# Performance work log

Hardware: AMD Instinct MI355X
Metric: run time of the kernel (lower is better)

Reference implementation:

```python
import jax, jax.numpy as jnp
import numpy as np

N_NODES = 50000
N_EDGES = 800000
D_IN = 96
D_OUT = 96


def setup_inputs() -> dict:
    key = jax.random.key(0)
    k1, k2, k3 = jax.random.split(key, 3)
    x = jax.random.normal(k1, (N_NODES, D_IN), dtype=jnp.float32)
    edge_index = jax.random.randint(k2, (2, N_EDGES), 0, N_NODES, dtype=jnp.int64)
    edge_weight = jnp.ones((N_EDGES,), dtype=jnp.float32)
    # Glorot-ish init for the linear weight, zero bias (as in PyG GCNConv)
    W = jax.random.normal(k3, (D_IN, D_OUT), dtype=jnp.float32) * (1.0 / np.sqrt(D_IN))
    b = jnp.zeros((D_OUT,), dtype=jnp.float32)
    return {"x": x, "edge_index": edge_index, "edge_weight": edge_weight, "W": W, "b": b}


def reference(x, edge_index, edge_weight, W, b):
    """PyG GCNConv: out = D^{-1/2} (A + I) D^{-1/2} (x @ W) + b."""
    N = x.shape[0]
    row, col = edge_index[0], edge_index[1]  # source -> target
    # add self loops with weight 1 (PyG default add_self_loops=True)
    loop = jnp.arange(N, dtype=edge_index.dtype)
    row = jnp.concatenate([row, loop])
    col = jnp.concatenate([col, loop])
    ew = jnp.concatenate([edge_weight, jnp.ones((N,), dtype=edge_weight.dtype)])
    # symmetric normalization based on (weighted) in-degree over col
    deg = jax.ops.segment_sum(ew, col, num_segments=N)  # [N]
    dinv = jnp.where(deg > 0, jax.lax.rsqrt(deg), 0.0)
    norm = dinv[row] * ew * dinv[col]  # [E+N]
    # linear transform first (small GEMM), then gather-scale-scatter over edges
    h = x @ W  # [N, D_OUT]
    msg = h[row] * norm[:, None]  # [E+N, D_OUT]
    out = jax.ops.segment_sum(msg, col, num_segments=N)  # [N, D_OUT]
    return out + b
```

## Files before the change

kernel.cpp:

```cpp
#include <hip/hip_runtime.h>

#define N_NODES 50000
#define N_EDGES 800000
#define D 96
#define NBKT 512
#define BNODES 98
#define BCAP 2304
#define PART_B 250
#define EPB 3200
#define EPT 13
#define CAP 48
#define NSLOT (BNODES * CAP)
#define GCAP 768

typedef float vfloat4 __attribute__((ext_vector_type(4)));

__device__ __forceinline__ float bf_lo(unsigned u) { return __uint_as_float(u << 16); }
__device__ __forceinline__ float bf_hi(unsigned u) { return __uint_as_float(u & 0xFFFF0000u); }
__device__ __forceinline__ unsigned f2bf_bits(unsigned u) {
    return (u + 0x7FFFu + ((u >> 16) & 1u)) & 0xFFFF0000u;
}
__device__ __forceinline__ unsigned short f2bf16(float f) {
    return (unsigned short)(f2bf_bits(__float_as_uint(f)) >> 16);
}

__device__ __forceinline__ int exscan256(int v, int* wsum) {
    int lane = threadIdx.x & 63;
    int wave = threadIdx.x >> 6;
    int incl = v;
#pragma unroll
    for (int off = 1; off < 64; off <<= 1) {
        int t = __shfl_up(incl, off);
        if (lane >= off) incl += t;
    }
    if (lane == 63) wsum[wave] = incl;
    __syncthreads();
    int base = 0;
#pragma unroll
    for (int wv = 0; wv < 3; ++wv) base += (wv < wave) ? wsum[wv] : 0;
    return base + incl - v;
}

__global__ __launch_bounds__(256) void k_part(const int* __restrict__ row,
                                              const int* __restrict__ col,
                                              const float* __restrict__ ew,
                                              int* __restrict__ bkt_cnt,
                                              uint2* __restrict__ bktbuf) {
    __shared__ int hist[NBKT];
    __shared__ int cur[NBKT];
    int tid = threadIdx.x;
    hist[tid] = 0;
    hist[tid + 256] = 0;
    __syncthreads();
    int e0 = blockIdx.x * EPB;
    int myc[EPT];
#pragma unroll
    for (int k = 0; k < EPT; ++k) {
        int i = tid + 256 * k;
        myc[k] = (i < EPB) ? col[e0 + i] : -1;
    }
#pragma unroll
    for (int k = 0; k < EPT; ++k)
        if (myc[k] >= 0) atomicAdd(&hist[myc[k] / BNODES], 1);
    __syncthreads();
    cur[tid] = atomicAdd(&bkt_cnt[tid], hist[tid]);
    cur[tid + 256] = atomicAdd(&bkt_cnt[tid + 256], hist[tid + 256]);
    __syncthreads();
#pragma unroll
    for (int k = 0; k < EPT; ++k) {
        int i = tid + 256 * k;
        if (myc[k] >= 0) {
            int e = e0 + i;
            int c = myc[k];
            int b = c / BNODES;
            int p = atomicAdd(&cur[b], 1);
            if (p < BCAP)
                bktbuf[(size_t)b * BCAP + p] =
                    make_uint2((unsigned)row[e] | ((unsigned)(c - b * BNODES) << 16),
                               __float_as_uint(ew[e]));
        }
    }
}

__global__ __launch_bounds__(256) void k_bin(const int* __restrict__ bkt_cnt,
                                             const uint2* __restrict__ bktbuf,
                                             unsigned* __restrict__ recs,
                                             int* __restrict__ rowptr,
                                             float* __restrict__ dinv) {
    __shared__ int wsum1[4];
    __shared__ int wsum2[4];
    __shared__ int sbkt[NBKT];
    __shared__ int lcnt[BNODES];
    __shared__ int loff[256];
    __shared__ unsigned lslot[NSLOT];
    int tid = threadIdx.x;
    int b = blockIdx.x;

    int c0 = min(bkt_cnt[2 * tid], BCAP);
    int c1 = min(bkt_cnt[2 * tid + 1], BCAP);
    int ps = exscan256(c0 + c1, wsum1);
    sbkt[2 * tid] = ps;
    sbkt[2 * tid + 1] = ps + c0;
    if (tid < BNODES) lcnt[tid] = 0;
    __syncthreads();
    int gbase = sbkt[b];
    int ne = min(bkt_cnt[b], BCAP);

    for (int i = tid; i < ne; i += 256) {
        uint2 r = bktbuf[(size_t)b * BCAP + i];
        int lc = (int)(r.x >> 16);
        int p = atomicAdd(&lcnt[lc], 1);
        if (p < CAP) lslot[lc * CAP + p] = f2bf_bits(r.y) | (r.x & 0xFFFFu);
    }
    __syncthreads();

    int myv = (tid < BNODES) ? min(lcnt[tid], CAP) : 0;
    int ex2 = exscan256(myv, wsum2);
    loff[tid] = ex2;
    __syncthreads();

    for (int i = tid; i < NSLOT; i += 256) {
        int ln = i / CAP, s = i % CAP;
        if (s < min(lcnt[ln], CAP))
            recs[gbase + loff[ln] + s] = lslot[i];
    }
    int base = b * BNODES;
    if (tid < BNODES) {
        int n = base + tid;
        if (n <= N_NODES) rowptr[n] = gbase + loff[tid];
        if (n < N_NODES) {
            int cn = min(lcnt[tid], CAP);
            float d = 1.0f;
            for (int k = 0; k < cn; ++k) d += bf_hi(lslot[tid * CAP + k]);
            dinv[n] = rsqrtf(d);
        }
    }
}

__global__ __launch_bounds__(256) void k_gemm(const float* __restrict__ x,
                                              const float* __restrict__ W,
                                              const float* __restrict__ dinv,
                                              unsigned short* __restrict__ hb) {
    __shared__ float Wl[D * D];
    int tid = threadIdx.x;
    const float4* Wg4 = (const float4*)W;
    float4* Wl4 = (float4*)Wl;
    for (int i = tid; i < D * D / 4; i += 256) Wl4[i] = Wg4[i];
    __syncthreads();

    int jg = tid % 24;
    int ng = tid / 24;
    if (ng >= 10) return;
    int j = jg * 4;
    int node0 = blockIdx.x * 40 + ng * 4;

    float acc[4][4] = {};
    for (int k4 = 0; k4 < D / 4; ++k4) {
        vfloat4 xv[4];
#pragma unroll
        for (int i = 0; i < 4; ++i)
            xv[i] = __builtin_nontemporal_load(
                (const vfloat4*)&x[(node0 + i) * D + k4 * 4]);
#pragma unroll
        for (int kk = 0; kk < 4; ++kk) {
            float4 w4 = *(const float4*)&Wl[(k4 * 4 + kk) * D + j];
#pragma unroll
            for (int i = 0; i < 4; ++i) {
                float xs = (kk == 0) ? xv[i].x : (kk == 1) ? xv[i].y
                         : (kk == 2) ? xv[i].z : xv[i].w;
                acc[i][0] += xs * w4.x;
                acc[i][1] += xs * w4.y;
                acc[i][2] += xs * w4.z;
                acc[i][3] += xs * w4.w;
            }
        }
    }
#pragma unroll
    for (int i = 0; i < 4; ++i) {
        int n = node0 + i;
        float di = dinv[n];
        ushort4 pk;
        pk.x = f2bf16(acc[i][0] * di);
        pk.y = f2bf16(acc[i][1] * di);
        pk.z = f2bf16(acc[i][2] * di);
        pk.w = f2bf16(acc[i][3] * di);
        *(ushort4*)&hb[(size_t)n * D + j] = pk;
    }
}

__global__ __launch_bounds__(192) void k_gather(const int* __restrict__ rowptr,
                                                const unsigned* __restrict__ recs,
                                                const unsigned short* __restrict__ hb,
                                                const float* __restrict__ dinv,
                                                const float* __restrict__ bias,
                                                float* __restrict__ out) {
    __shared__ unsigned sre[GCAP];
    __shared__ int sptr[17];
    int tid = threadIdx.x;
    int nb = blockIdx.x * 16;

    if (tid < 17) sptr[tid] = rowptr[nb + tid];
    __syncthreads();
    int e0 = sptr[0];
    int stage = sptr[16] - e0;
    for (int i = tid; i < stage; i += 192) sre[i] = recs[e0 + i];
    __syncthreads();

    int local = tid / 12;
    int jq = tid % 12;
    int n = nb + local;
    int j = jq * 8;

    uint4 sv = *(const uint4*)(hb + (size_t)n * D + j);
    float acc[8];
    acc[0] = bf_lo(sv.x); acc[1] = bf_hi(sv.x);
    acc[2] = bf_lo(sv.y); acc[3] = bf_hi(sv.y);
    acc[4] = bf_lo(sv.z); acc[5] = bf_hi(sv.z);
    acc[6] = bf_lo(sv.w); acc[7] = bf_hi(sv.w);

    int ls = sptr[local] - e0;
    int le = sptr[local + 1] - e0;
    int idx = ls;
    for (; idx + 4 <= le; idx += 4) {
        unsigned r0 = sre[idx], r1 = sre[idx + 1], r2 = sre[idx + 2], r3 = sre[idx + 3];
        uint4 v0 = *(const uint4*)(hb + (size_t)(r0 & 0xFFFFu) * D + j);
        uint4 v1 = *(const uint4*)(hb + (size_t)(r1 & 0xFFFFu) * D + j);
        uint4 v2 = *(const uint4*)(hb + (size_t)(r2 & 0xFFFFu) * D + j);
        uint4 v3 = *(const uint4*)(hb + (size_t)(r3 & 0xFFFFu) * D + j);
        float w0 = bf_hi(r0), w1 = bf_hi(r1), w2 = bf_hi(r2), w3 = bf_hi(r3);
        acc[0] += w0 * bf_lo(v0.x); acc[1] += w0 * bf_hi(v0.x);
        acc[2] += w0 * bf_lo(v0.y); acc[3] += w0 * bf_hi(v0.y);
        acc[4] += w0 * bf_lo(v0.z); acc[5] += w0 * bf_hi(v0.z);
        acc[6] += w0 * bf_lo(v0.w); acc[7] += w0 * bf_hi(v0.w);
        acc[0] += w1 * bf_lo(v1.x); acc[1] += w1 * bf_hi(v1.x);
        acc[2] += w1 * bf_lo(v1.y); acc[3] += w1 * bf_hi(v1.y);
        acc[4] += w1 * bf_lo(v1.z); acc[5] += w1 * bf_hi(v1.z);
        acc[6] += w1 * bf_lo(v1.w); acc[7] += w1 * bf_hi(v1.w);
        acc[0] += w2 * bf_lo(v2.x); acc[1] += w2 * bf_hi(v2.x);
        acc[2] += w2 * bf_lo(v2.y); acc[3] += w2 * bf_hi(v2.y);
        acc[4] += w2 * bf_lo(v2.z); acc[5] += w2 * bf_hi(v2.z);
        acc[6] += w2 * bf_lo(v2.w); acc[7] += w2 * bf_hi(v2.w);
        acc[0] += w3 * bf_lo(v3.x); acc[1] += w3 * bf_hi(v3.x);
        acc[2] += w3 * bf_lo(v3.y); acc[3] += w3 * bf_hi(v3.y);
        acc[4] += w3 * bf_lo(v3.z); acc[5] += w3 * bf_hi(v3.z);
        acc[6] += w3 * bf_lo(v3.w); acc[7] += w3 * bf_hi(v3.w);
    }
    for (; idx < le; ++idx) {
        unsigned r0 = sre[idx];
        uint4 v0 = *(const uint4*)(hb + (size_t)(r0 & 0xFFFFu) * D + j);
        float w0 = bf_hi(r0);
        acc[0] += w0 * bf_lo(v0.x); acc[1] += w0 * bf_hi(v0.x);
        acc[2] += w0 * bf_lo(v0.y); acc[3] += w0 * bf_hi(v0.y);
        acc[4] += w0 * bf_lo(v0.z); acc[5] += w0 * bf_hi(v0.z);
        acc[6] += w0 * bf_lo(v0.w); acc[7] += w0 * bf_hi(v0.w);
    }

    float di = dinv[n];
    float4 b0 = *(const float4*)&bias[j];
    float4 b1 = *(const float4*)&bias[j + 4];
    vfloat4 o0, o1;
    o0.x = acc[0] * di + b0.x; o0.y = acc[1] * di + b0.y;
    o0.z = acc[2] * di + b0.z; o0.w = acc[3] * di + b0.w;
    o1.x = acc[4] * di + b1.x; o1.y = acc[5] * di + b1.y;
    o1.z = acc[6] * di + b1.z; o1.w = acc[7] * di + b1.w;
    __builtin_nontemporal_store(o0, (vfloat4*)&out[(size_t)n * D + j]);
    __builtin_nontemporal_store(o1, (vfloat4*)&out[(size_t)n * D + j + 4]);
}

extern "C" void kernel_launch(void* const* d_in, const int* in_sizes, int n_in,
                              void* d_out, int out_size, void* d_ws, size_t ws_size,
                              hipStream_t stream) {
    const float* x  = (const float*)d_in[0];
    const int*   ei = (const int*)d_in[1];
    const float* ew = (const float*)d_in[2];
    const float* W  = (const float*)d_in[3];
    const float* b  = (const float*)d_in[4];
    float* out = (float*)d_out;

    const int* row = ei;
    const int* col = ei + N_EDGES;

    char* p = (char*)d_ws;
    unsigned short* hb     = (unsigned short*)p;
    uint2*          bktbuf = (uint2*)p;            p += (size_t)N_NODES * D * 2;
    unsigned*       recs   = (unsigned*)p;         p += (size_t)N_EDGES * 4;
    int*            rowptr = (int*)p;              p += (size_t)(N_NODES + 16) * 4;
    float*          dinv   = (float*)p;            p += (size_t)N_NODES * 4;
    int*            bkt_cnt= (int*)p;              p += (size_t)NBKT * 4;

    (void)hipMemsetAsync(bkt_cnt, 0, NBKT * sizeof(int), stream);
    k_part  <<<PART_B, 256, 0, stream>>>(row, col, ew, bkt_cnt, bktbuf);
    k_bin   <<<NBKT, 256, 0, stream>>>(bkt_cnt, bktbuf, recs, rowptr, dinv);
    k_gemm  <<<1250, 256, 0, stream>>>(x, W, dinv, hb);
    k_gather<<<(N_NODES + 15) / 16, 192, 0, stream>>>(rowptr, recs, hb, dinv, b, out);
}
```

Before: 152.8 us.

## Stage partition writes in LDS by bucket and sort gather nodes by degree

The partition kernel now builds a local exclusive scan of the bucket histogram and writes each edge record into shared memory grouped by bucket. It then flushes the staged records so that consecutive threads write contiguous global bucket slots, in place of scattered per-edge writes. The gather kernel ranks its 16 nodes by degree so that wavefronts handle nodes of similar edge counts, which is meant to cut divergence from uneven loop trip counts. The cost is about 25KB of extra LDS in the partition kernel, which may lower occupancy, plus an extra barrier and a small ranking step.

```diff
diff --git a/kernel.cpp b/kernel.cpp
--- a/kernel.cpp
+++ b/kernel.cpp
@@ -47,7 +47,11 @@
                                               int* __restrict__ bkt_cnt,
                                               uint2* __restrict__ bktbuf) {
     __shared__ int hist[NBKT];
-    __shared__ int cur[NBKT];
+    __shared__ int lbase[NBKT];
+    __shared__ int gcur[NBKT];
+    __shared__ int lcur[NBKT];
+    __shared__ int wsum[4];
+    __shared__ uint2 stg[EPB];
     int tid = threadIdx.x;
     hist[tid] = 0;
     hist[tid + 256] = 0;
@@ -63,8 +67,15 @@
     for (int k = 0; k < EPT; ++k)
         if (myc[k] >= 0) atomicAdd(&hist[myc[k] / BNODES], 1);
     __syncthreads();
-    cur[tid] = atomicAdd(&bkt_cnt[tid], hist[tid]);
-    cur[tid + 256] = atomicAdd(&bkt_cnt[tid + 256], hist[tid + 256]);
+    int c0 = hist[2 * tid];
+    int c1 = hist[2 * tid + 1];
+    int ps = exscan256(c0 + c1, wsum);
+    lbase[2 * tid] = ps;
+    lbase[2 * tid + 1] = ps + c0;
+    lcur[2 * tid] = ps;
+    lcur[2 * tid + 1] = ps + c0;
+    gcur[2 * tid] = atomicAdd(&bkt_cnt[2 * tid], c0);
+    gcur[2 * tid + 1] = atomicAdd(&bkt_cnt[2 * tid + 1], c1);
     __syncthreads();
 #pragma unroll
     for (int k = 0; k < EPT; ++k) {
@@ -73,12 +84,19 @@
             int e = e0 + i;
             int c = myc[k];
             int b = c / BNODES;
-            int p = atomicAdd(&cur[b], 1);
-            if (p < BCAP)
-                bktbuf[(size_t)b * BCAP + p] =
-                    make_uint2((unsigned)row[e] | ((unsigned)(c - b * BNODES) << 16),
-                               __float_as_uint(ew[e]));
+            int p = atomicAdd(&lcur[b], 1);
+            stg[p] = make_uint2((unsigned)row[e] | ((unsigned)(c - b * BNODES) << 16) |
+                                    ((unsigned)b << 23),
+                                __float_as_uint(ew[e]));
         }
+    }
+    __syncthreads();
+    for (int i = tid; i < EPB; i += 256) {
+        uint2 r = stg[i];
+        int b = (int)(r.x >> 23);
+        int pos = gcur[b] + (i - lbase[b]);
+        if (pos < BCAP)
+            bktbuf[(size_t)b * BCAP + pos] = make_uint2(r.x & 0x7FFFFFu, r.y);
     }
 }
 
@@ -196,19 +214,30 @@
                                                 float* __restrict__ out) {
     __shared__ unsigned sre[GCAP];
     __shared__ int sptr[17];
+    __shared__ unsigned char perm[16];
     int tid = threadIdx.x;
     int nb = blockIdx.x * 16;
 
     if (tid < 17) sptr[tid] = rowptr[nb + tid];
     __syncthreads();
+    if (tid < 16) {
+        int di = sptr[tid + 1] - sptr[tid];
+        int rank = 0;
+#pragma unroll
+        for (int jn = 0; jn < 16; ++jn) {
+            int dj = sptr[jn + 1] - sptr[jn];
+            rank += (dj > di) || (dj == di && jn < tid);
+        }
+        perm[rank] = (unsigned char)tid;
+    }
     int e0 = sptr[0];
     int stage = sptr[16] - e0;
     for (int i = tid; i < stage; i += 192) sre[i] = recs[e0 + i];
     __syncthreads();
 
-    int local = tid / 12;
+    int pl = perm[tid / 12];
     int jq = tid % 12;
-    int n = nb + local;
+    int n = nb + pl;
     int j = jq * 8;
 
     uint4 sv = *(const uint4*)(hb + (size_t)n * D + j);
@@ -218,8 +247,8 @@
     acc[4] = bf_lo(sv.z); acc[5] = bf_hi(sv.z);
     acc[6] = bf_lo(sv.w); acc[7] = bf_hi(sv.w);
 
-    int ls = sptr[local] - e0;
-    int le = sptr[local + 1] - e0;
+    int ls = sptr[pl] - e0;
+    int le = sptr[pl + 1] - e0;
     int idx = ls;
     for (; idx + 4 <= le; idx += 4) {
         unsigned r0 = sre[idx], r1 = sre[idx + 1], r2 = sre[idx + 2], r3 = sre[idx + 3];
```

Result: slower. 157.1 us (+2.8%).

## Fuse pipeline into one cooperative persistent kernel with grid syncs

Applied to the files above, without the earlier changes.

Replaces the four launches (partition, bin, GEMM, gather) with one cooperative kernel of 1024 blocks separated by grid-wide syncs. The binning and the x@W GEMM now run concurrently on disjoint block sets, so the GEMM no longer waits on dinv: dinv scaling moves into the gather, where per-edge weights are pre-multiplied by dinv[src] when staged in shared memory. The gather also sorts the nodes of each tile by degree to balance its waves. In exchange it pays grid-sync costs and a larger shared-memory union that may limit occupancy, and it falls back to three normal launches if the cooperative launch fails.

```diff
diff --git a/kernel.cpp b/kernel.cpp
--- a/kernel.cpp
+++ b/kernel.cpp
@@ -1,4 +1,7 @@
 #include <hip/hip_runtime.h>
+#include <hip/hip_cooperative_groups.h>
+
+namespace cg = cooperative_groups;
 
 #define N_NODES 50000
 #define N_EDGES 800000
@@ -6,12 +9,13 @@
 #define NBKT 512
 #define BNODES 98
 #define BCAP 2304
-#define PART_B 250
-#define EPB 3200
-#define EPT 13
 #define CAP 48
 #define NSLOT (BNODES * CAP)
-#define GCAP 768
+#define GRID 1024
+#define NTILE 21
+#define PCAP (NTILE * CAP)
+#define NTILES ((N_NODES + NTILE - 1) / NTILE)
+#define NVB 1250
 
 typedef float vfloat4 __attribute__((ext_vector_type(4)));
 
@@ -41,230 +45,259 @@
     return base + incl - v;
 }
 
-__global__ __launch_bounds__(256) void k_part(const int* __restrict__ row,
-                                              const int* __restrict__ col,
-                                              const float* __restrict__ ew,
-                                              int* __restrict__ bkt_cnt,
-                                              uint2* __restrict__ bktbuf) {
-    __shared__ int hist[NBKT];
-    __shared__ int cur[NBKT];
+union __align__(16) SMem {
+    struct { int hist[NBKT]; int cur[NBKT]; } p1;
+    struct {
+        int sbkt[NBKT]; int lcnt[BNODES]; int loff[256];
+        unsigned lslot[NSLOT]; int wsum1[4]; int wsum2[4];
+    } p2b;
+    struct { float Wl[D * D]; } p2g;
+    struct {
+        int sptr[NTILE + 1]; uint2 sed[PCAP]; unsigned char perm[NTILE];
+    } p3;
+};
+
+__global__ __launch_bounds__(256, 4) void k_fused(
+    const int* __restrict__ row, const int* __restrict__ col,
+    const float* __restrict__ ew, const float* __restrict__ x,
+    const float* __restrict__ W, const float* __restrict__ bias,
+    int* __restrict__ bkt_cnt, uint2* __restrict__ bktbuf,
+    unsigned* __restrict__ recs, int* __restrict__ rowptr,
+    float* __restrict__ dinv, unsigned short* __restrict__ hb,
+    float* __restrict__ out, int phase) {
+    __shared__ SMem sm;
     int tid = threadIdx.x;
-    hist[tid] = 0;
-    hist[tid + 256] = 0;
-    __syncthreads();
-    int e0 = blockIdx.x * EPB;
-    int myc[EPT];
-#pragma unroll
-    for (int k = 0; k < EPT; ++k) {
-        int i = tid + 256 * k;
-        myc[k] = (i < EPB) ? col[e0 + i] : -1;
-    }
-#pragma unroll
-    for (int k = 0; k < EPT; ++k)
-        if (myc[k] >= 0) atomicAdd(&hist[myc[k] / BNODES], 1);
-    __syncthreads();
-    cur[tid] = atomicAdd(&bkt_cnt[tid], hist[tid]);
-    cur[tid + 256] = atomicAdd(&bkt_cnt[tid + 256], hist[tid + 256]);
-    __syncthreads();
-#pragma unroll
-    for (int k = 0; k < EPT; ++k) {
-        int i = tid + 256 * k;
-        if (myc[k] >= 0) {
-            int e = e0 + i;
-            int c = myc[k];
-            int b = c / BNODES;
-            int p = atomicAdd(&cur[b], 1);
-            if (p < BCAP)
-                bktbuf[(size_t)b * BCAP + p] =
-                    make_uint2((unsigned)row[e] | ((unsigned)(c - b * BNODES) << 16),
-                               __float_as_uint(ew[e]));
-        }
-    }
-}
-
-__global__ __launch_bounds__(256) void k_bin(const int* __restrict__ bkt_cnt,
-                                             const uint2* __restrict__ bktbuf,
-                                             unsigned* __restrict__ recs,
-                                             int* __restrict__ rowptr,
-                                             float* __restrict__ dinv) {
-    __shared__ int wsum1[4];
-    __shared__ int wsum2[4];
-    __shared__ int sbkt[NBKT];
-    __shared__ int lcnt[BNODES];
-    __shared__ int loff[256];
-    __shared__ unsigned lslot[NSLOT];
-    int tid = threadIdx.x;
-    int b = blockIdx.x;
-
-    int c0 = min(bkt_cnt[2 * tid], BCAP);
-    int c1 = min(bkt_cnt[2 * tid + 1], BCAP);
-    int ps = exscan256(c0 + c1, wsum1);
-    sbkt[2 * tid] = ps;
-    sbkt[2 * tid + 1] = ps + c0;
-    if (tid < BNODES) lcnt[tid] = 0;
-    __syncthreads();
-    int gbase = sbkt[b];
-    int ne = min(bkt_cnt[b], BCAP);
-
-    for (int i = tid; i < ne; i += 256) {
-        uint2 r = bktbuf[(size_t)b * BCAP + i];
-        int lc = (int)(r.x >> 16);
-        int p = atomicAdd(&lcnt[lc], 1);
-        if (p < CAP) lslot[lc * CAP + p] = f2bf_bits(r.y) | (r.x & 0xFFFFu);
-    }
-    __syncthreads();
-
-    int myv = (tid < BNODES) ? min(lcnt[tid], CAP) : 0;
-    int ex2 = exscan256(myv, wsum2);
-    loff[tid] = ex2;
-    __syncthreads();
-
-    for (int i = tid; i < NSLOT; i += 256) {
-        int ln = i / CAP, s = i % CAP;
-        if (s < min(lcnt[ln], CAP))
-            recs[gbase + loff[ln] + s] = lslot[i];
-    }
-    int base = b * BNODES;
-    if (tid < BNODES) {
-        int n = base + tid;
-        if (n <= N_NODES) rowptr[n] = gbase + loff[tid];
-        if (n < N_NODES) {
-            int cn = min(lcnt[tid], CAP);
-            float d = 1.0f;
-            for (int k = 0; k < cn; ++k) d += bf_hi(lslot[tid * CAP + k]);
-            dinv[n] = rsqrtf(d);
-        }
-    }
-}
-
-__global__ __launch_bounds__(256) void k_gemm(const float* __restrict__ x,
-                                              const float* __restrict__ W,
-                                              const float* __restrict__ dinv,
-                                              unsigned short* __restrict__ hb) {
-    __shared__ float Wl[D * D];
-    int tid = threadIdx.x;
-    const float4* Wg4 = (const float4*)W;
-    float4* Wl4 = (float4*)Wl;
-    for (int i = tid; i < D * D / 4; i += 256) Wl4[i] = Wg4[i];
-    __syncthreads();
-
-    int jg = tid % 24;
-    int ng = tid / 24;
-    if (ng >= 10) return;
-    int j = jg * 4;
-    int node0 = blockIdx.x * 40 + ng * 4;
-
-    float acc[4][4] = {};
-    for (int k4 = 0; k4 < D / 4; ++k4) {
-        vfloat4 xv[4];
-#pragma unroll
-        for (int i = 0; i < 4; ++i)
-            xv[i] = __builtin_nontemporal_load(
-                (const vfloat4*)&x[(node0 + i) * D + k4 * 4]);
-#pragma unroll
-        for (int kk = 0; kk < 4; ++kk) {
-            float4 w4 = *(const float4*)&Wl[(k4 * 4 + kk) * D + j];
-#pragma unroll
-            for (int i = 0; i < 4; ++i) {
-                float xs = (kk == 0) ? xv[i].x : (kk == 1) ? xv[i].y
-                         : (kk == 2) ? xv[i].z : xv[i].w;
-                acc[i][0] += xs * w4.x;
-                acc[i][1] += xs * w4.y;
-                acc[i][2] += xs * w4.z;
-                acc[i][3] += xs * w4.w;
-            }
-        }
-    }
-#pragma unroll
-    for (int i = 0; i < 4; ++i) {
-        int n = node0 + i;
-        float di = dinv[n];
-        ushort4 pk;
-        pk.x = f2bf16(acc[i][0] * di);
-        pk.y = f2bf16(acc[i][1] * di);
-        pk.z = f2bf16(acc[i][2] * di);
-        pk.w = f2bf16(acc[i][3] * di);
-        *(ushort4*)&hb[(size_t)n * D + j] = pk;
-    }
-}
-
-__global__ __launch_bounds__(192) void k_gather(const int* __restrict__ rowptr,
-                                                const unsigned* __restrict__ recs,
-                                                const unsigned short* __restrict__ hb,
-                                                const float* __restrict__ dinv,
-                                                const float* __restrict__ bias,
-                                                float* __restrict__ out) {
-    __shared__ unsigned sre[GCAP];
-    __shared__ int sptr[17];
-    int tid = threadIdx.x;
-    int nb = blockIdx.x * 16;
-
-    if (tid < 17) sptr[tid] = rowptr[nb + tid];
-    __syncthreads();
-    int e0 = sptr[0];
-    int stage = sptr[16] - e0;
-    for (int i = tid; i < stage; i += 192) sre[i] = recs[e0 + i];
-    __syncthreads();
-
-    int local = tid / 12;
-    int jq = tid % 12;
-    int n = nb + local;
-    int j = jq * 8;
-
-    uint4 sv = *(const uint4*)(hb + (size_t)n * D + j);
-    float acc[8];
-    acc[0] = bf_lo(sv.x); acc[1] = bf_hi(sv.x);
-    acc[2] = bf_lo(sv.y); acc[3] = bf_hi(sv.y);
-    acc[4] = bf_lo(sv.z); acc[5] = bf_hi(sv.z);
-    acc[6] = bf_lo(sv.w); acc[7] = bf_hi(sv.w);
-
-    int ls = sptr[local] - e0;
-    int le = sptr[local + 1] - e0;
-    int idx = ls;
-    for (; idx + 4 <= le; idx += 4) {
-        unsigned r0 = sre[idx], r1 = sre[idx + 1], r2 = sre[idx + 2], r3 = sre[idx + 3];
-        uint4 v0 = *(const uint4*)(hb + (size_t)(r0 & 0xFFFFu) * D + j);
-        uint4 v1 = *(const uint4*)(hb + (size_t)(r1 & 0xFFFFu) * D + j);
-        uint4 v2 = *(const uint4*)(hb + (size_t)(r2 & 0xFFFFu) * D + j);
-        uint4 v3 = *(const uint4*)(hb + (size_t)(r3 & 0xFFFFu) * D + j);
-        float w0 = bf_hi(r0), w1 = bf_hi(r1), w2 = bf_hi(r2), w3 = bf_hi(r3);
-        acc[0] += w0 * bf_lo(v0.x); acc[1] += w0 * bf_hi(v0.x);
-        acc[2] += w0 * bf_lo(v0.y); acc[3] += w0 * bf_hi(v0.y);
-        acc[4] += w0 * bf_lo(v0.z); acc[5] += w0 * bf_hi(v0.z);
-        acc[6] += w0 * bf_lo(v0.w); acc[7] += w0 * bf_hi(v0.w);
-        acc[0] += w1 * bf_lo(v1.x); acc[1] += w1 * bf_hi(v1.x);
-        acc[2] += w1 * bf_lo(v1.y); acc[3] += w1 * bf_hi(v1.y);
-        acc[4] += w1 * bf_lo(v1.z); acc[5] += w1 * bf_hi(v1.z);
-        acc[6] += w1 * bf_lo(v1.w); acc[7] += w1 * bf_hi(v1.w);
-        acc[0] += w2 * bf_lo(v2.x); acc[1] += w2 * bf_hi(v2.x);
-        acc[2] += w2 * bf_lo(v2.y); acc[3] += w2 * bf_hi(v2.y);
-        acc[4] += w2 * bf_lo(v2.z); acc[5] += w2 * bf_hi(v2.z);
-        acc[6] += w2 * bf_lo(v2.w); acc[7] += w2 * bf_hi(v2.w);
-        acc[0] += w3 * bf_lo(v3.x); acc[1] += w3 * bf_hi(v3.x);
-        acc[2] += w3 * bf_lo(v3.y); acc[3] += w3 * bf_hi(v3.y);
-        acc[4] += w3 * bf_lo(v3.z); acc[5] += w3 * bf_hi(v3.z);
-        acc[6] += w3 * bf_lo(v3.w); acc[7] += w3 * bf_hi(v3.w);
-    }
-    for (; idx < le; ++idx) {
-        unsigned r0 = sre[idx];
-        uint4 v0 = *(const uint4*)(hb + (size_t)(r0 & 0xFFFFu) * D + j);
-        float w0 = bf_hi(r0);
-        acc[0] += w0 * bf_lo(v0.x); acc[1] += w0 * bf_hi(v0.x);
-        acc[2] += w0 * bf_lo(v0.y); acc[3] += w0 * bf_hi(v0.y);
-        acc[4] += w0 * bf_lo(v0.z); acc[5] += w0 * bf_hi(v0.z);
-        acc[6] += w0 * bf_lo(v0.w); acc[7] += w0 * bf_hi(v0.w);
-    }
-
-    float di = dinv[n];
-    float4 b0 = *(const float4*)&bias[j];
-    float4 b1 = *(const float4*)&bias[j + 4];
-    vfloat4 o0, o1;
-    o0.x = acc[0] * di + b0.x; o0.y = acc[1] * di + b0.y;
-    o0.z = acc[2] * di + b0.z; o0.w = acc[3] * di + b0.w;
-    o1.x = acc[4] * di + b1.x; o1.y = acc[5] * di + b1.y;
-    o1.z = acc[6] * di + b1.z; o1.w = acc[7] * di + b1.w;
-    __builtin_nontemporal_store(o0, (vfloat4*)&out[(size_t)n * D + j]);
-    __builtin_nontemporal_store(o1, (vfloat4*)&out[(size_t)n * D + j + 4]);
+    int bid = blockIdx.x;
+
+    if (phase <= 1) {
+        int* hist = sm.p1.hist;
+        int* cur = sm.p1.cur;
+        hist[tid] = 0;
+        hist[tid + 256] = 0;
+        __syncthreads();
+        int e0 = (bid * N_EDGES) / GRID;
+        int e1 = ((bid + 1) * N_EDGES) / GRID;
+        int myc[4];
+#pragma unroll
+        for (int k = 0; k < 4; ++k) {
+            int e = e0 + tid + 256 * k;
+            myc[k] = (e < e1) ? col[e] : -1;
+        }
+#pragma unroll
+        for (int k = 0; k < 4; ++k)
+            if (myc[k] >= 0) atomicAdd(&hist[myc[k] / BNODES], 1);
+        __syncthreads();
+        {
+            int h0 = hist[tid], h1 = hist[tid + 256];
+            cur[tid] = h0 ? atomicAdd(&bkt_cnt[tid], h0) : 0;
+            cur[tid + 256] = h1 ? atomicAdd(&bkt_cnt[tid + 256], h1) : 0;
+        }
+        __syncthreads();
+#pragma unroll
+        for (int k = 0; k < 4; ++k) {
+            if (myc[k] >= 0) {
+                int e = e0 + tid + 256 * k;
+                int c = myc[k];
+                int b = c / BNODES;
+                int p = atomicAdd(&cur[b], 1);
+                if (p < BCAP)
+                    bktbuf[(size_t)b * BCAP + p] =
+                        make_uint2((unsigned)row[e] | ((unsigned)(c - b * BNODES) << 16),
+                                   __float_as_uint(ew[e]));
+            }
+        }
+    }
+    if (phase == 0) cg::this_grid().sync();
+
+    if (phase == 0 || phase == 2) {
+        if (bid < NBKT) {
+            int* sbkt = sm.p2b.sbkt;
+            int* lcnt = sm.p2b.lcnt;
+            int* loff = sm.p2b.loff;
+            unsigned* lslot = sm.p2b.lslot;
+            int c0 = min(bkt_cnt[2 * tid], BCAP);
+            int c1 = min(bkt_cnt[2 * tid + 1], BCAP);
+            int ps = exscan256(c0 + c1, sm.p2b.wsum1);
+            sbkt[2 * tid] = ps;
+            sbkt[2 * tid + 1] = ps + c0;
+            if (tid < BNODES) lcnt[tid] = 0;
+            __syncthreads();
+            int gbase = sbkt[bid];
+            int ne = min(bkt_cnt[bid], BCAP);
+
+            for (int i = tid; i < ne; i += 256) {
+                uint2 r = bktbuf[(size_t)bid * BCAP + i];
+                int lc = (int)(r.x >> 16);
+                int p = atomicAdd(&lcnt[lc], 1);
+                if (p < CAP) lslot[lc * CAP + p] = f2bf_bits(r.y) | (r.x & 0xFFFFu);
+            }
+            __syncthreads();
+
+            int myv = (tid < BNODES) ? min(lcnt[tid], CAP) : 0;
+            int ex2 = exscan256(myv, sm.p2b.wsum2);
+            loff[tid] = ex2;
+            __syncthreads();
+
+            for (int i = tid; i < NSLOT; i += 256) {
+                int ln = i / CAP, s = i % CAP;
+                if (s < min(lcnt[ln], CAP))
+                    recs[gbase + loff[ln] + s] = lslot[i];
+            }
+            int base = bid * BNODES;
+            if (tid < BNODES) {
+                int n = base + tid;
+                if (n <= N_NODES) rowptr[n] = gbase + loff[tid];
+                if (n < N_NODES) {
+                    int cn = min(lcnt[tid], CAP);
+                    float d = 1.0f;
+                    for (int k = 0; k < cn; ++k) d += bf_hi(lslot[tid * CAP + k]);
+                    dinv[n] = rsqrtf(d);
+                }
+            }
+        } else {
+            float* Wl = sm.p2g.Wl;
+            const float4* Wg4 = (const float4*)W;
+            float4* Wl4 = (float4*)Wl;
+            for (int i = tid; i < D * D / 4; i += 256) Wl4[i] = Wg4[i];
+            __syncthreads();
+            int jg = tid % 24;
+            int ng = tid / 24;
+            for (int vb = bid - NBKT; vb < NVB; vb += (GRID - NBKT)) {
+                if (ng < 10) {
+                    int j = jg * 4;
+                    int node0 = vb * 40 + ng * 4;
+                    float acc[4][4] = {};
+                    for (int k4 = 0; k4 < D / 4; ++k4) {
+                        vfloat4 xv[4];
+#pragma unroll
+                        for (int i = 0; i < 4; ++i)
+                            xv[i] = __builtin_nontemporal_load(
+                                (const vfloat4*)&x[(node0 + i) * D + k4 * 4]);
+#pragma unroll
+                        for (int kk = 0; kk < 4; ++kk) {
+                            float4 w4 = *(const float4*)&Wl[(k4 * 4 + kk) * D + j];
+#pragma unroll
+                            for (int i = 0; i < 4; ++i) {
+                                float xs = (kk == 0) ? xv[i].x : (kk == 1) ? xv[i].y
+                                         : (kk == 2) ? xv[i].z : xv[i].w;
+                                acc[i][0] += xs * w4.x;
+                                acc[i][1] += xs * w4.y;
+                                acc[i][2] += xs * w4.z;
+                                acc[i][3] += xs * w4.w;
+                            }
+                        }
+                    }
+#pragma unroll
+                    for (int i = 0; i < 4; ++i) {
+                        ushort4 pk;
+                        pk.x = f2bf16(acc[i][0]);
+                        pk.y = f2bf16(acc[i][1]);
+                        pk.z = f2bf16(acc[i][2]);
+                        pk.w = f2bf16(acc[i][3]);
+                        *(ushort4*)&hb[(size_t)(node0 + i) * D + j] = pk;
+                    }
+                }
+            }
+        }
+    }
+    if (phase == 0) cg::this_grid().sync();
+
+    if (phase == 0 || phase == 3) {
+        int* sptr = sm.p3.sptr;
+        uint2* sed = sm.p3.sed;
+        unsigned char* perm = sm.p3.perm;
+        int lg = tid / 12;
+        int jq = tid % 12;
+        int j = jq * 8;
+        for (int t = bid; t < NTILES; t += GRID) {
+            __syncthreads();
+            int nb = t * NTILE;
+            if (tid <= NTILE) sptr[tid] = rowptr[min(nb + tid, N_NODES)];
+            __syncthreads();
+            if (tid < NTILE) {
+                int dmy = sptr[tid + 1] - sptr[tid];
+                int rank = 0;
+#pragma unroll
+                for (int jn = 0; jn < NTILE; ++jn) {
+                    int dj = sptr[jn + 1] - sptr[jn];
+                    rank += (dj > dmy) || (dj == dmy && jn < tid);
+                }
+                perm[rank] = (unsigned char)tid;
+            }
+            int e0 = sptr[0];
+            int stage = sptr[NTILE] - e0;
+            for (int i = tid; i < stage; i += 256) {
+                unsigned r = recs[e0 + i];
+                int src = (int)(r & 0xFFFFu);
+                sed[i] = make_uint2((unsigned)src,
+                                    __float_as_uint(bf_hi(r) * dinv[src]));
+            }
+            __syncthreads();
+
+            int pl = (lg < NTILE) ? perm[lg] : 0;
+            int n = nb + pl;
+            bool act = (lg < NTILE) && (n < N_NODES);
+            float acc[8] = {};
+            float di = 0.f;
+            if (act) {
+                di = dinv[n];
+                uint4 sv = *(const uint4*)(hb + (size_t)n * D + j);
+                acc[0] = bf_lo(sv.x) * di; acc[1] = bf_hi(sv.x) * di;
+                acc[2] = bf_lo(sv.y) * di; acc[3] = bf_hi(sv.y) * di;
+                acc[4] = bf_lo(sv.z) * di; acc[5] = bf_hi(sv.z) * di;
+                acc[6] = bf_lo(sv.w) * di; acc[7] = bf_hi(sv.w) * di;
+            }
+            int ls = act ? (sptr[pl] - e0) : 0;
+            int le = act ? (sptr[pl + 1] - e0) : 0;
+            int idx = ls;
+            for (; idx + 4 <= le; idx += 4) {
+                uint2 ed0 = sed[idx], ed1 = sed[idx + 1];
+                uint2 ed2 = sed[idx + 2], ed3 = sed[idx + 3];
+                uint4 v0 = *(const uint4*)(hb + (size_t)ed0.x * D + j);
+                uint4 v1 = *(const uint4*)(hb + (size_t)ed1.x * D + j);
+                uint4 v2 = *(const uint4*)(hb + (size_t)ed2.x * D + j);
+                uint4 v3 = *(const uint4*)(hb + (size_t)ed3.x * D + j);
+                float w0 = __uint_as_float(ed0.y), w1 = __uint_as_float(ed1.y);
+                float w2 = __uint_as_float(ed2.y), w3 = __uint_as_float(ed3.y);
+                acc[0] += w0 * bf_lo(v0.x); acc[1] += w0 * bf_hi(v0.x);
+                acc[2] += w0 * bf_lo(v0.y); acc[3] += w0 * bf_hi(v0.y);
+                acc[4] += w0 * bf_lo(v0.z); acc[5] += w0 * bf_hi(v0.z);
+                acc[6] += w0 * bf_lo(v0.w); acc[7] += w0 * bf_hi(v0.w);
+                acc[0] += w1 * bf_lo(v1.x); acc[1] += w1 * bf_hi(v1.x);
+                acc[2] += w1 * bf_lo(v1.y); acc[3] += w1 * bf_hi(v1.y);
+                acc[4] += w1 * bf_lo(v1.z); acc[5] += w1 * bf_hi(v1.z);
+                acc[6] += w1 * bf_lo(v1.w); acc[7] += w1 * bf_hi(v1.w);
+                acc[0] += w2 * bf_lo(v2.x); acc[1] += w2 * bf_hi(v2.x);
+                acc[2] += w2 * bf_lo(v2.y); acc[3] += w2 * bf_hi(v2.y);
+                acc[4] += w2 * bf_lo(v2.z); acc[5] += w2 * bf_hi(v2.z);
+                acc[6] += w2 * bf_lo(v2.w); acc[7] += w2 * bf_hi(v2.w);
+                acc[0] += w3 * bf_lo(v3.x); acc[1] += w3 * bf_hi(v3.x);
+                acc[2] += w3 * bf_lo(v3.y); acc[3] += w3 * bf_hi(v3.y);
+                acc[4] += w3 * bf_lo(v3.z); acc[5] += w3 * bf_hi(v3.z);
+                acc[6] += w3 * bf_lo(v3.w); acc[7] += w3 * bf_hi(v3.w);
+            }
+            for (; idx < le; ++idx) {
+                uint2 ed = sed[idx];
+                uint4 v0 = *(const uint4*)(hb + (size_t)ed.x * D + j);
+                float w0 = __uint_as_float(ed.y);
+                acc[0] += w0 * bf_lo(v0.x); acc[1] += w0 * bf_hi(v0.x);
+                acc[2] += w0 * bf_lo(v0.y); acc[3] += w0 * bf_hi(v0.y);
+                acc[4] += w0 * bf_lo(v0.z); acc[5] += w0 * bf_hi(v0.z);
+                acc[6] += w0 * bf_lo(v0.w); acc[7] += w0 * bf_hi(v0.w);
+            }
+            if (act) {
+                float4 b0 = *(const float4*)&bias[j];
+                float4 b1 = *(const float4*)&bias[j + 4];
+                vfloat4 o0, o1;
+                o0.x = acc[0] * di + b0.x; o0.y = acc[1] * di + b0.y;
+                o0.z = acc[2] * di + b0.z; o0.w = acc[3] * di + b0.w;
+                o1.x = acc[4] * di + b1.x; o1.y = acc[5] * di + b1.y;
+                o1.z = acc[6] * di + b1.z; o1.w = acc[7] * di + b1.w;
+                __builtin_nontemporal_store(o0, (vfloat4*)&out[(size_t)n * D + j]);
+                __builtin_nontemporal_store(o1, (vfloat4*)&out[(size_t)n * D + j + 4]);
+            }
+        }
+    }
 }
 
 extern "C" void kernel_launch(void* const* d_in, const int* in_sizes, int n_in,
@@ -281,16 +314,31 @@
     const int* col = ei + N_EDGES;
 
     char* p = (char*)d_ws;
-    unsigned short* hb     = (unsigned short*)p;
-    uint2*          bktbuf = (uint2*)p;            p += (size_t)N_NODES * D * 2;
+    unsigned short* hb     = (unsigned short*)p;   p += (size_t)N_NODES * D * 2;
+    uint2*          bktbuf = (uint2*)p;            p += (size_t)NBKT * BCAP * 8;
     unsigned*       recs   = (unsigned*)p;         p += (size_t)N_EDGES * 4;
-    int*            rowptr = (int*)p;              p += (size_t)(N_NODES + 16) * 4;
+    int*            rowptr = (int*)p;              p += (size_t)(N_NODES + 64) * 4;
     float*          dinv   = (float*)p;            p += (size_t)N_NODES * 4;
     int*            bkt_cnt= (int*)p;              p += (size_t)NBKT * 4;
 
     (void)hipMemsetAsync(bkt_cnt, 0, NBKT * sizeof(int), stream);
-    k_part  <<<PART_B, 256, 0, stream>>>(row, col, ew, bkt_cnt, bktbuf);
-    k_bin   <<<NBKT, 256, 0, stream>>>(bkt_cnt, bktbuf, recs, rowptr, dinv);
-    k_gemm  <<<1250, 256, 0, stream>>>(x, W, dinv, hb);
-    k_gather<<<(N_NODES + 15) / 16, 192, 0, stream>>>(rowptr, recs, hb, dinv, b, out);
-}
+
+    int phase = 0;
+    void* args[] = {(void*)&row, (void*)&col, (void*)&ew, (void*)&x, (void*)&W,
+                    (void*)&b, (void*)&bkt_cnt, (void*)&bktbuf, (void*)&recs,
+                    (void*)&rowptr, (void*)&dinv, (void*)&hb, (void*)&out,
+                    (void*)&phase};
+    hipError_t err = hipLaunchCooperativeKernel((const void*)k_fused, dim3(GRID),
+                                                dim3(256), args, 0u, stream);
+    if (err != hipSuccess) {
+        hipLaunchKernelGGL(k_fused, dim3(GRID), dim3(256), 0, stream,
+                           row, col, ew, x, W, b, bkt_cnt, bktbuf, recs,
+                           rowptr, dinv, hb, out, 1);
+        hipLaunchKernelGGL(k_fused, dim3(GRID), dim3(256), 0, stream,
+                           row, col, ew, x, W, b, bkt_cnt, bktbuf, recs,
+                           rowptr, dinv, hb, out, 2);
+        hipLaunchKernelGGL(k_fused, dim3(GRID), dim3(256), 0, stream,
+                           row, col, ew, x, W, b, bkt_cnt, bktbuf, recs,
+                           rowptr, dinv, hb, out, 3);
+    }
+}
```

After: 456.5 us. 2.99x slower.

## Fuse edge partition with GEMM and move source normalization into gather

Applied to the files above, without the earlier changes.

Merges the edge-bucketing kernel and the x@W GEMM into one launch whose blocks are split by blockIdx. This lets the GEMM run concurrently with partitioning instead of waiting for dinv. The source-side dinv scaling leaves the GEMM: each edge weight is premultiplied by dinv[src] while staging in the gather kernel. hb and bktbuf no longer alias, so workspace use grows. The gather also sorts its 16 nodes by degree so that waves get balanced work, at the cost of an extra dinv gather per edge.

```diff
diff --git a/kernel.cpp b/kernel.cpp
--- a/kernel.cpp
+++ b/kernel.cpp
@@ -12,6 +12,7 @@
 #define CAP 48
 #define NSLOT (BNODES * CAP)
 #define GCAP 768
+#define GEMM_B 1250
 
 typedef float vfloat4 __attribute__((ext_vector_type(4)));
 
@@ -41,43 +42,99 @@
     return base + incl - v;
 }
 
-__global__ __launch_bounds__(256) void k_part(const int* __restrict__ row,
-                                              const int* __restrict__ col,
-                                              const float* __restrict__ ew,
-                                              int* __restrict__ bkt_cnt,
-                                              uint2* __restrict__ bktbuf) {
-    __shared__ int hist[NBKT];
-    __shared__ int cur[NBKT];
+union __align__(16) SMemPG {
+    struct { int hist[NBKT]; int cur[NBKT]; } p;
+    float Wl[D * D];
+};
+
+__global__ __launch_bounds__(256) void k_partgemm(
+    const int* __restrict__ row, const int* __restrict__ col,
+    const float* __restrict__ ew, const float* __restrict__ x,
+    const float* __restrict__ W, int* __restrict__ bkt_cnt,
+    uint2* __restrict__ bktbuf, unsigned short* __restrict__ hb) {
+    __shared__ SMemPG sm;
     int tid = threadIdx.x;
-    hist[tid] = 0;
-    hist[tid + 256] = 0;
-    __syncthreads();
-    int e0 = blockIdx.x * EPB;
-    int myc[EPT];
-#pragma unroll
-    for (int k = 0; k < EPT; ++k) {
-        int i = tid + 256 * k;
-        myc[k] = (i < EPB) ? col[e0 + i] : -1;
-    }
-#pragma unroll
-    for (int k = 0; k < EPT; ++k)
-        if (myc[k] >= 0) atomicAdd(&hist[myc[k] / BNODES], 1);
-    __syncthreads();
-    cur[tid] = atomicAdd(&bkt_cnt[tid], hist[tid]);
-    cur[tid + 256] = atomicAdd(&bkt_cnt[tid + 256], hist[tid + 256]);
-    __syncthreads();
-#pragma unroll
-    for (int k = 0; k < EPT; ++k) {
-        int i = tid + 256 * k;
-        if (myc[k] >= 0) {
-            int e = e0 + i;
-            int c = myc[k];
-            int b = c / BNODES;
-            int p = atomicAdd(&cur[b], 1);
-            if (p < BCAP)
-                bktbuf[(size_t)b * BCAP + p] =
-                    make_uint2((unsigned)row[e] | ((unsigned)(c - b * BNODES) << 16),
-                               __float_as_uint(ew[e]));
+    int bid = blockIdx.x;
+
+    if (bid < PART_B) {
+        int* hist = sm.p.hist;
+        int* cur = sm.p.cur;
+        hist[tid] = 0;
+        hist[tid + 256] = 0;
+        __syncthreads();
+        int e0 = bid * EPB;
+        int myc[EPT];
+#pragma unroll
+        for (int k = 0; k < EPT; ++k) {
+            int i = tid + 256 * k;
+            myc[k] = (i < EPB) ? col[e0 + i] : -1;
+        }
+#pragma unroll
+        for (int k = 0; k < EPT; ++k)
+            if (myc[k] >= 0) atomicAdd(&hist[myc[k] / BNODES], 1);
+        __syncthreads();
+        {
+            int h0 = hist[tid], h1 = hist[tid + 256];
+            cur[tid] = h0 ? atomicAdd(&bkt_cnt[tid], h0) : 0;
+            cur[tid + 256] = h1 ? atomicAdd(&bkt_cnt[tid + 256], h1) : 0;
+        }
+        __syncthreads();
+#pragma unroll
+        for (int k = 0; k < EPT; ++k) {
+            int i = tid + 256 * k;
+            if (myc[k] >= 0) {
+                int e = e0 + i;
+                int c = myc[k];
+                int b = c / BNODES;
+                int p = atomicAdd(&cur[b], 1);
+                if (p < BCAP)
+                    bktbuf[(size_t)b * BCAP + p] =
+                        make_uint2((unsigned)row[e] | ((unsigned)(c - b * BNODES) << 16),
+                                   __float_as_uint(ew[e]));
+            }
+        }
+    } else {
+        float* Wl = sm.Wl;
+        const float4* Wg4 = (const float4*)W;
+        float4* Wl4 = (float4*)Wl;
+        for (int i = tid; i < D * D / 4; i += 256) Wl4[i] = Wg4[i];
+        __syncthreads();
+
+        int jg = tid % 24;
+        int ng = tid / 24;
+        if (ng < 10) {
+            int j = jg * 4;
+            int node0 = (bid - PART_B) * 40 + ng * 4;
+            float acc[4][4] = {};
+            for (int k4 = 0; k4 < D / 4; ++k4) {
+                vfloat4 xv[4];
+#pragma unroll
+                for (int i = 0; i < 4; ++i)
+                    xv[i] = __builtin_nontemporal_load(
+                        (const vfloat4*)&x[(node0 + i) * D + k4 * 4]);
+#pragma unroll
+                for (int kk = 0; kk < 4; ++kk) {
+                    float4 w4 = *(const float4*)&Wl[(k4 * 4 + kk) * D + j];
+#pragma unroll
+                    for (int i = 0; i < 4; ++i) {
+                        float xs = (kk == 0) ? xv[i].x : (kk == 1) ? xv[i].y
+                                 : (kk == 2) ? xv[i].z : xv[i].w;
+                        acc[i][0] += xs * w4.x;
+                        acc[i][1] += xs * w4.y;
+                        acc[i][2] += xs * w4.z;
+                        acc[i][3] += xs * w4.w;
+                    }
+                }
+            }
+#pragma unroll
+            for (int i = 0; i < 4; ++i) {
+                ushort4 pk;
+                pk.x = f2bf16(acc[i][0]);
+                pk.y = f2bf16(acc[i][1]);
+                pk.z = f2bf16(acc[i][2]);
+                pk.w = f2bf16(acc[i][3]);
+                *(ushort4*)&hb[(size_t)(node0 + i) * D + j] = pk;
+            }
         }
     }
 }
@@ -137,97 +194,65 @@
     }
 }
 
-__global__ __launch_bounds__(256) void k_gemm(const float* __restrict__ x,
-                                              const float* __restrict__ W,
-                                              const float* __restrict__ dinv,
-                                              unsigned short* __restrict__ hb) {
-    __shared__ float Wl[D * D];
-    int tid = threadIdx.x;
-    const float4* Wg4 = (const float4*)W;
-    float4* Wl4 = (float4*)Wl;
-    for (int i = tid; i < D * D / 4; i += 256) Wl4[i] = Wg4[i];
-    __syncthreads();
-
-    int jg = tid % 24;
-    int ng = tid / 24;
-    if (ng >= 10) return;
-    int j = jg * 4;
-    int node0 = blockIdx.x * 40 + ng * 4;
-
-    float acc[4][4] = {};
-    for (int k4 = 0; k4 < D / 4; ++k4) {
-        vfloat4 xv[4];
-#pragma unroll
-        for (int i = 0; i < 4; ++i)
-            xv[i] = __builtin_nontemporal_load(
-                (const vfloat4*)&x[(node0 + i) * D + k4 * 4]);
-#pragma unroll
-        for (int kk = 0; kk < 4; ++kk) {
-            float4 w4 = *(const float4*)&Wl[(k4 * 4 + kk) * D + j];
-#pragma unroll
-            for (int i = 0; i < 4; ++i) {
-                float xs = (kk == 0) ? xv[i].x : (kk == 1) ? xv[i].y
-                         : (kk == 2) ? xv[i].z : xv[i].w;
-                acc[i][0] += xs * w4.x;
-                acc[i][1] += xs * w4.y;
-                acc[i][2] += xs * w4.z;
-                acc[i][3] += xs * w4.w;
-            }
-        }
-    }
-#pragma unroll
-    for (int i = 0; i < 4; ++i) {
-        int n = node0 + i;
-        float di = dinv[n];
-        ushort4 pk;
-        pk.x = f2bf16(acc[i][0] * di);
-        pk.y = f2bf16(acc[i][1] * di);
-        pk.z = f2bf16(acc[i][2] * di);
-        pk.w = f2bf16(acc[i][3] * di);
-        *(ushort4*)&hb[(size_t)n * D + j] = pk;
-    }
-}
-
 __global__ __launch_bounds__(192) void k_gather(const int* __restrict__ rowptr,
                                                 const unsigned* __restrict__ recs,
                                                 const unsigned short* __restrict__ hb,
                                                 const float* __restrict__ dinv,
                                                 const float* __restrict__ bias,
                                                 float* __restrict__ out) {
-    __shared__ unsigned sre[GCAP];
+    __shared__ uint2 sed[GCAP];
     __shared__ int sptr[17];
+    __shared__ unsigned char perm[16];
     int tid = threadIdx.x;
     int nb = blockIdx.x * 16;
 
     if (tid < 17) sptr[tid] = rowptr[nb + tid];
     __syncthreads();
+    if (tid < 16) {
+        int dmy = sptr[tid + 1] - sptr[tid];
+        int rank = 0;
+#pragma unroll
+        for (int jn = 0; jn < 16; ++jn) {
+            int dj = sptr[jn + 1] - sptr[jn];
+            rank += (dj > dmy) || (dj == dmy && jn < tid);
+        }
+        perm[rank] = (unsigned char)tid;
+    }
     int e0 = sptr[0];
     int stage = sptr[16] - e0;
-    for (int i = tid; i < stage; i += 192) sre[i] = recs[e0 + i];
-    __syncthreads();
-
-    int local = tid / 12;
+    for (int i = tid; i < stage; i += 192) {
+        unsigned r = recs[e0 + i];
+        int src = (int)(r & 0xFFFFu);
+        sed[i] = make_uint2((unsigned)src,
+                            __float_as_uint(bf_hi(r) * dinv[src]));
+    }
+    __syncthreads();
+
+    int pl = perm[tid / 12];
     int jq = tid % 12;
-    int n = nb + local;
+    int n = nb + pl;
     int j = jq * 8;
 
+    float di = dinv[n];
     uint4 sv = *(const uint4*)(hb + (size_t)n * D + j);
     float acc[8];
-    acc[0] = bf_lo(sv.x); acc[1] = bf_hi(sv.x);
-    acc[2] = bf_lo(sv.y); acc[3] = bf_hi(sv.y);
-    acc[4] = bf_lo(sv.z); acc[5] = bf_hi(sv.z);
-    acc[6] = bf_lo(sv.w); acc[7] = bf_hi(sv.w);
-
-    int ls = sptr[local] - e0;
-    int le = sptr[local + 1] - e0;
+    acc[0] = bf_lo(sv.x) * di; acc[1] = bf_hi(sv.x) * di;
+    acc[2] = bf_lo(sv.y) * di; acc[3] = bf_hi(sv.y) * di;
+    acc[4] = bf_lo(sv.z) * di; acc[5] = bf_hi(sv.z) * di;
+    acc[6] = bf_lo(sv.w) * di; acc[7] = bf_hi(sv.w) * di;
+
+    int ls = sptr[pl] - e0;
+    int le = sptr[pl + 1] - e0;
     int idx = ls;
     for (; idx + 4 <= le; idx += 4) {
-        unsigned r0 = sre[idx], r1 = sre[idx + 1], r2 = sre[idx + 2], r3 = sre[idx + 3];
-        uint4 v0 = *(const uint4*)(hb + (size_t)(r0 & 0xFFFFu) * D + j);
-        uint4 v1 = *(const uint4*)(hb + (size_t)(r1 & 0xFFFFu) * D + j);
-        uint4 v2 = *(const uint4*)(hb + (size_t)(r2 & 0xFFFFu) * D + j);
-        uint4 v3 = *(const uint4*)(hb + (size_t)(r3 & 0xFFFFu) * D + j);
-        float w0 = bf_hi(r0), w1 = bf_hi(r1), w2 = bf_hi(r2), w3 = bf_hi(r3);
+        uint2 e0r = sed[idx], e1r = sed[idx + 1];
+        uint2 e2r = sed[idx + 2], e3r = sed[idx + 3];
+        uint4 v0 = *(const uint4*)(hb + (size_t)e0r.x * D + j);
+        uint4 v1 = *(const uint4*)(hb + (size_t)e1r.x * D + j);
+        uint4 v2 = *(const uint4*)(hb + (size_t)e2r.x * D + j);
+        uint4 v3 = *(const uint4*)(hb + (size_t)e3r.x * D + j);
+        float w0 = __uint_as_float(e0r.y), w1 = __uint_as_float(e1r.y);
+        float w2 = __uint_as_float(e2r.y), w3 = __uint_as_float(e3r.y);
         acc[0] += w0 * bf_lo(v0.x); acc[1] += w0 * bf_hi(v0.x);
         acc[2] += w0 * bf_lo(v0.y); acc[3] += w0 * bf_hi(v0.y);
         acc[4] += w0 * bf_lo(v0.z); acc[5] += w0 * bf_hi(v0.z);
@@ -246,16 +271,15 @@
         acc[6] += w3 * bf_lo(v3.w); acc[7] += w3 * bf_hi(v3.w);
     }
     for (; idx < le; ++idx) {
-        unsigned r0 = sre[idx];
-        uint4 v0 = *(const uint4*)(hb + (size_t)(r0 & 0xFFFFu) * D + j);
-        float w0 = bf_hi(r0);
+        uint2 er = sed[idx];
+        uint4 v0 = *(const uint4*)(hb + (size_t)er.x * D + j);
+        float w0 = __uint_as_float(er.y);
         acc[0] += w0 * bf_lo(v0.x); acc[1] += w0 * bf_hi(v0.x);
         acc[2] += w0 * bf_lo(v0.y); acc[3] += w0 * bf_hi(v0.y);
         acc[4] += w0 * bf_lo(v0.z); acc[5] += w0 * bf_hi(v0.z);
         acc[6] += w0 * bf_lo(v0.w); acc[7] += w0 * bf_hi(v0.w);
     }
 
-    float di = dinv[n];
     float4 b0 = *(const float4*)&bias[j];
     float4 b1 = *(const float4*)&bias[j + 4];
     vfloat4 o0, o1;
@@ -281,16 +305,16 @@
     const int* col = ei + N_EDGES;
 
     char* p = (char*)d_ws;
-    unsigned short* hb     = (unsigned short*)p;
-    uint2*          bktbuf = (uint2*)p;            p += (size_t)N_NODES * D * 2;
+    unsigned short* hb     = (unsigned short*)p;   p += (size_t)N_NODES * D * 2;
+    uint2*          bktbuf = (uint2*)p;            p += (size_t)NBKT * BCAP * 8;
     unsigned*       recs   = (unsigned*)p;         p += (size_t)N_EDGES * 4;
-    int*            rowptr = (int*)p;              p += (size_t)(N_NODES + 16) * 4;
+    int*            rowptr = (int*)p;              p += (size_t)(N_NODES + 64) * 4;
     float*          dinv   = (float*)p;            p += (size_t)N_NODES * 4;
     int*            bkt_cnt= (int*)p;              p += (size_t)NBKT * 4;
 
     (void)hipMemsetAsync(bkt_cnt, 0, NBKT * sizeof(int), stream);
-    k_part  <<<PART_B, 256, 0, stream>>>(row, col, ew, bkt_cnt, bktbuf);
+    k_partgemm<<<PART_B + GEMM_B, 256, 0, stream>>>(row, col, ew, x, W,
+                                                    bkt_cnt, bktbuf, hb);
     k_bin   <<<NBKT, 256, 0, stream>>>(bkt_cnt, bktbuf, recs, rowptr, dinv);
-    k_gemm  <<<1250, 256, 0, stream>>>(x, W, dinv, hb);
     k_gather<<<(N_NODES + 15) / 16, 192, 0, stream>>>(rowptr, recs, hb, dinv, b, out);
 }
```

New measurement: 152.1 us. Within noise of the previous version (-0.5%).
